# Kernel optimization log

Hardware: AMD Instinct MI355X
Metric: run time of the kernel (lower is better)

The kernel has to match this reference:

```python
import jax, jax.numpy as jnp
import numpy as np

NS, NV = 32, 8                      # scalar / vector multiplicities (32x0e + 8x1o)
N_NODES, N_EDGES = 16384, 131072
NEF, HID = 128, 128                 # edge feature dim, MLP hidden
WN = NS*NS + NV*NS + NS*NV + NV*NV  # 1600 tensor-product weights per edge
D = NS + 3*NV                       # 56 node feature dim
INV_SQRT3 = 1.0/np.sqrt(3.0)        # CG coeff for 1o x 1o -> 0e
PATH_NORM = 1.0/np.sqrt(NS + NV)    # fan-in normalization per output irrep
EPS = 1e-5


def setup_inputs() -> dict:
    key = jax.random.key(0)
    ks = jax.random.split(key, 10)
    node_attr = jax.random.normal(ks[0], (N_NODES, D), jnp.float32)
    edge_index = jax.random.randint(ks[1], (2, N_EDGES), 0, N_NODES, dtype=jnp.int64)
    edge_attr = jax.random.normal(ks[2], (N_EDGES, NEF), jnp.float32)
    edge_sh = jax.random.normal(ks[3], (N_EDGES, 4), jnp.float32)
    W1 = jax.random.normal(ks[4], (NEF, HID), jnp.float32) / np.sqrt(NEF)
    b1 = jnp.zeros((HID,), jnp.float32)
    W2 = jax.random.normal(ks[5], (HID, WN), jnp.float32) / np.sqrt(HID)
    b2 = jnp.zeros((WN,), jnp.float32)
    bn_gamma = jnp.ones((NS + NV,), jnp.float32)   # per-irrep scale (scalars then vectors)
    bn_beta = jnp.zeros((NS,), jnp.float32)        # bias only on scalar irreps
    return dict(node_attr=node_attr, edge_attr=edge_attr, edge_sh=edge_sh,
                W1=W1, b1=b1, W2=W2, b2=b2, bn_gamma=bn_gamma, bn_beta=bn_beta,
                edge_index=edge_index)


def reference(node_attr, edge_attr, edge_sh, W1, b1, W2, b2, bn_gamma, bn_beta, edge_index):
    edge_src, edge_dst = edge_index[0], edge_index[1]

    # per-edge tensor-product weights from edge MLP (dropout=0, eval mode)
    w = jax.nn.relu(edge_attr @ W1 + b1) @ W2 + b2            # [E, WN]
    o0 = NS*NS; o1 = o0 + NV*NS; o2 = o1 + NS*NV
    w_ss = w[:, :o0].reshape(-1, NS, NS)   # 0e x 0e -> 0e
    w_vs = w[:, o0:o1].reshape(-1, NV, NS) # 1o x 1o -> 0e
    w_sv = w[:, o1:o2].reshape(-1, NS, NV) # 0e x 1o -> 1o
    w_vv = w[:, o2:].reshape(-1, NV, NV)   # 1o x 0e -> 1o

    # gather node features onto edges
    x = node_attr[edge_dst]                # [E, D]
    xs = x[:, :NS]                         # [E, NS]
    xv = x[:, NS:].reshape(-1, NV, 3)      # [E, NV, 3]
    ss = edge_sh[:, 0]                     # [E]
    sv = edge_sh[:, 1:4]                   # [E, 3]

    # CG tensor product with per-edge fully-connected weights
    dot_vv = jnp.einsum('eim,em->ei', xv, sv) * INV_SQRT3
    out_s = (jnp.einsum('eij,ei->ej', w_ss, xs) * ss[:, None]
             + jnp.einsum('eij,ei->ej', w_vs, dot_vv)) * PATH_NORM          # [E, NS]
    out_v = (jnp.einsum('eij,ei->ej', w_sv, xs)[:, :, None] * sv[:, None, :]
             + jnp.einsum('eij,eim->ejm', w_vv, xv) * ss[:, None, None]) * PATH_NORM  # [E, NV, 3]
    tp = jnp.concatenate([out_s, out_v.reshape(-1, 3*NV)], axis=-1)         # [E, D]

    # scatter-mean to source nodes
    sums = jax.ops.segment_sum(tp, edge_src, num_segments=N_NODES)
    cnt = jax.ops.segment_sum(jnp.ones((tp.shape[0], 1), tp.dtype), edge_src,
                              num_segments=N_NODES)
    out = sums / jnp.maximum(cnt, 1.0)

    # residual (in/out irreps identical -> zero padding is a no-op)
    out = out + node_attr

    # equivariant batch norm (training-mode batch statistics)
    s = out[:, :NS]
    v = out[:, NS:].reshape(-1, NV, 3)
    s = (s - s.mean(0)) / jnp.sqrt(s.var(0) + EPS) * bn_gamma[:NS] + bn_beta
    vn2 = (v * v).sum(-1).mean(0)                               # [NV] mean squared norm
    v = v / jnp.sqrt(vn2 + EPS)[None, :, None] * bn_gamma[NS:][None, :, None]
    return jnp.concatenate([s, v.reshape(-1, 3*NV)], axis=-1)
```

## Files before the change

### kernel.cpp

```cpp
#include <hip/hip_runtime.h>

typedef short short8 __attribute__((ext_vector_type(8)));
typedef unsigned short us4 __attribute__((ext_vector_type(4)));
typedef float floatx4 __attribute__((ext_vector_type(4)));
typedef unsigned short u16;

#define NN 16384
#define NE 131072
#define NEF_ 128
#define DD 56
#define INV_SQRT3F 0.57735026918962576f
#define PATH_NORMF 0.15811388300841897f

__device__ __forceinline__ float bf2f(u16 u) {
    union { unsigned int i; float f; } v; v.i = ((unsigned int)u) << 16; return v.f;
}
__device__ __forceinline__ u16 f2bf(float f) {
    union { float f; unsigned int i; } v; v.f = f;
    unsigned int r = v.i + 0x7fffu + ((v.i >> 16) & 1u);
    return (u16)(r >> 16);
}

__global__ __launch_bounds__(256) void prep(const float* __restrict__ W1,
                                            const float* __restrict__ W2,
                                            u16* __restrict__ W1f,
                                            u16* __restrict__ W2f,
                                            const int* __restrict__ eidx,
                                            int* __restrict__ deg) {
    int b = blockIdx.x;
    if (b < 864) {
        int i = b * 256 + threadIdx.x;
        if (i < 16384) {
            int cc = i >> 13, kk = (i >> 11) & 3, cg = (i >> 9) & 3;
            int lane = (i >> 3) & 63, j = i & 7;
            int q = lane >> 4, m = lane & 15;
            W1f[i] = f2bf(W1[(kk * 32 + q * 8 + j) * 128 + cc * 64 + cg * 16 + m]);
        } else {
            int f = i - 16384;
            int c = f >> 13, kk = (f >> 11) & 3, cg = (f >> 9) & 3;
            int lane = (f >> 3) & 63, j = f & 7;
            int q = lane >> 4, m = lane & 15;
            W2f[f] = f2bf(W2[(kk * 32 + q * 8 + j) * 1600 + c * 64 + cg * 16 + m]);
        }
    } else {
        int e = (b - 864) * 256 + threadIdx.x;
        atomicAdd(&deg[eidx[e]], 1);
    }
}

__global__ __launch_bounds__(1024) void deg_scan(const int* __restrict__ deg,
                                                 int* __restrict__ row_start,
                                                 int* __restrict__ cursor) {
    __shared__ int part[1024];
    const int t = threadIdx.x;
    const int base = t * 16;
    int loc[16];
    int s = 0;
    #pragma unroll
    for (int i = 0; i < 16; i++) { loc[i] = s; s += deg[base + i]; }
    part[t] = s;
    __syncthreads();
    for (int off = 1; off < 1024; off <<= 1) {
        int v = (t >= off) ? part[t - off] : 0;
        __syncthreads();
        part[t] += v;
        __syncthreads();
    }
    int pre = (t == 0) ? 0 : part[t - 1];
    #pragma unroll
    for (int i = 0; i < 16; i++) {
        int v = pre + loc[i];
        row_start[base + i] = v;
        cursor[base + i] = v;
    }
    if (t == 1023) row_start[16384] = pre + s;
}

__global__ __launch_bounds__(256) void edge_scatter(const int* __restrict__ eidx,
                                                    int* __restrict__ cursor,
                                                    int* __restrict__ edge_order) {
    int e = blockIdx.x * 256 + threadIdx.x;
    int p = atomicAdd(&cursor[eidx[e]], 1);
    edge_order[p] = e;
}

__global__ __launch_bounds__(512, 4) void tpconv(
    const float* __restrict__ node_attr, const float* __restrict__ edge_attr,
    const float* __restrict__ edge_sh, const u16* __restrict__ W1f,
    const float* __restrict__ b1, const u16* __restrict__ W2f,
    const float* __restrict__ b2, const int* __restrict__ eidx,
    const int* __restrict__ edge_order,
    float* __restrict__ tp)
{
    __shared__ __align__(16) char smem[48896];
    u16*   sA  = (u16*)smem;
    u16*   B2a = (u16*)(smem + 17408);
    u16*   B2b = (u16*)smem;
    u16*   sF  = (u16*)(smem + 33792);
    float* b2s = (float*)(smem + 42496);
    float* Ssc  = (float*)smem;
    float* Svec = (float*)(smem + 16896);

    const int t = threadIdx.x;
    const int lane = t & 63;
    const int wv = t >> 6;
    const int m = lane & 15;
    const int q = lane >> 4;
    const int cg = wv & 3;
    const int eh = wv >> 2;
    const int eb = eh * 32;
    const int p0 = blockIdx.x * 64;

    short8 pre[2];
    #pragma unroll
    for (int ii = 0; ii < 2; ii++)
        pre[ii] = *(const short8*)&W2f[ii * 4096 + t * 8];

    for (int i = t; i < 1600; i += 512) b2s[i] = b2[i];

    #pragma unroll
    for (int ii = 0; ii < 4; ii++) {
        int cid = t + 512 * ii;
        int r = cid >> 5, s = cid & 31;
        int e = edge_order[p0 + r];
        const float* src = &edge_attr[(size_t)e * NEF_ + s * 4];
        us4 o;
        o.x = f2bf(src[0]); o.y = f2bf(src[1]); o.z = f2bf(src[2]); o.w = f2bf(src[3]);
        *(us4*)&sA[r * 136 + s * 4] = o;
    }
    if (t < 64) {
        int e = edge_order[p0 + t];
        int nd = eidx[NE + e];
        const float* na = node_attr + (size_t)nd * DD;
        const float* sh = edge_sh + (size_t)e * 4;
        float ss = sh[0], s0 = sh[1], s1 = sh[2], s2 = sh[3];
        #pragma unroll
        for (int i = 0; i < 32; i++) sF[i * 64 + t] = f2bf(na[i]);
        #pragma unroll
        for (int i = 0; i < 8; i++) {
            float d = (na[32+i*3]*s0 + na[33+i*3]*s1 + na[34+i*3]*s2) * INV_SQRT3F;
            sF[(32 + i) * 64 + t] = f2bf(d);
        }
        #pragma unroll
        for (int i = 0; i < 24; i++) sF[(40 + i) * 64 + t] = f2bf(na[32 + i]);
        sF[64 * 64 + t] = f2bf(ss);
        sF[65 * 64 + t] = f2bf(s0);
        sF[66 * 64 + t] = f2bf(s1);
        sF[67 * 64 + t] = f2bf(s2);
    }
    __syncthreads();

    floatx4 hacc[2][2];
    #pragma unroll
    for (int cc = 0; cc < 2; cc++) {
        #pragma unroll
        for (int ii = 0; ii < 2; ii++)
            *(short8*)&B2a[ii * 4096 + t * 8] =
                *(const short8*)&W1f[cc * 8192 + ii * 4096 + t * 8];
        __syncthreads();
        {
            float bv = b1[cc * 64 + cg * 16 + m];
            hacc[cc][0] = (floatx4){bv, bv, bv, bv};
            hacc[cc][1] = hacc[cc][0];
        }
        #pragma unroll
        for (int kk = 0; kk < 4; kk++) {
            short8 a0 = *(const short8*)&sA[(eb      + m) * 136 + kk * 32 + q * 8];
            short8 a1 = *(const short8*)&sA[(eb + 16 + m) * 136 + kk * 32 + q * 8];
            short8 bA = *(const short8*)&B2a[(kk * 4 + cg) * 512 + lane * 8];
            hacc[cc][0] = __builtin_amdgcn_mfma_f32_16x16x32_bf16(a0, bA, hacc[cc][0], 0, 0, 0);
            hacc[cc][1] = __builtin_amdgcn_mfma_f32_16x16x32_bf16(a1, bA, hacc[cc][1], 0, 0, 0);
        }
        __syncthreads();
    }
    #pragma unroll
    for (int cc = 0; cc < 2; cc++)
      #pragma unroll
      for (int rt = 0; rt < 2; rt++)
        #pragma unroll
        for (int r = 0; r < 4; r++) {
            int e   = eb + rt * 16 + q * 4 + r;
            int col = cc * 64 + cg * 16 + m;
            float v = hacc[cc][rt][r];
            sA[e * 136 + col] = f2bf(v > 0.f ? v : 0.f);
        }
    __syncthreads();

    short8 hc[2][4];
    #pragma unroll
    for (int et = 0; et < 2; et++)
        #pragma unroll
        for (int kk = 0; kk < 4; kk++)
            hc[et][kk] = *(const short8*)&sA[(eb + et * 16 + m) * 136 + kk * 32 + q * 8];

    float ssc[2], svc[2][3];
    #pragma unroll
    for (int et = 0; et < 2; et++) {
        ssc[et] = bf2f(sF[64 * 64 + eb + et * 16 + m]);
        svc[et][0] = bf2f(sF[65 * 64 + eb + et * 16 + m]);
        svc[et][1] = bf2f(sF[66 * 64 + eb + et * 16 + m]);
        svc[et][2] = bf2f(sF[67 * 64 + eb + et * 16 + m]);
    }

    #pragma unroll
    for (int ii = 0; ii < 2; ii++)
        *(short8*)&B2a[ii * 4096 + t * 8] = pre[ii];
    #pragma unroll
    for (int ii = 0; ii < 2; ii++)
        pre[ii] = *(const short8*)&W2f[8192 + ii * 4096 + t * 8];
    __syncthreads();

    float tps[2][4];
    float tpv[2][4][3];
    #pragma unroll
    for (int et = 0; et < 2; et++)
        #pragma unroll
        for (int r = 0; r < 4; r++) {
            tps[et][r] = 0.f;
            tpv[et][r][0] = 0.f; tpv[et][r][1] = 0.f; tpv[et][r][2] = 0.f;
        }

    for (int c = 0; c < 25; c++) {
        const u16* rb = (c & 1) ? B2b : B2a;
        u16*       wb = (c & 1) ? B2a : B2b;

        floatx4 bias = *(const floatx4*)&b2s[c * 64 + cg * 16 + q * 4];
        floatx4 acc[2];
        acc[0] = bias; acc[1] = bias;
        #pragma unroll
        for (int kk = 0; kk < 4; kk++) {
            short8 a = *(const short8*)&rb[(kk * 4 + cg) * 512 + lane * 8];
            acc[0] = __builtin_amdgcn_mfma_f32_16x16x32_bf16(a, hc[0][kk], acc[0], 0, 0, 0);
            acc[1] = __builtin_amdgcn_mfma_f32_16x16x32_bf16(a, hc[1][kk], acc[1], 0, 0, 0);
        }

        if (c < 24) {
            #pragma unroll
            for (int ii = 0; ii < 2; ii++)
                *(short8*)&wb[ii * 4096 + t * 8] = pre[ii];
            if (c < 23) {
                #pragma unroll
                for (int ii = 0; ii < 2; ii++)
                    pre[ii] = *(const short8*)&W2f[(size_t)(c + 2) * 8192 + ii * 4096 + t * 8];
            }
        }

        if (c < 16) {
            const int i = 2 * c + (cg >> 1);
            #pragma unroll
            for (int et = 0; et < 2; et++) {
                float f = bf2f(sF[i * 64 + eb + et * 16 + m]) * ssc[et];
                #pragma unroll
                for (int r = 0; r < 4; r++) tps[et][r] += acc[et][r] * f;
            }
        } else if (c < 20) {
            const int i = 2 * (c - 16) + (cg >> 1);
            #pragma unroll
            for (int et = 0; et < 2; et++) {
                float f = bf2f(sF[(32 + i) * 64 + eb + et * 16 + m]);
                #pragma unroll
                for (int r = 0; r < 4; r++) tps[et][r] += acc[et][r] * f;
            }
        } else if (c < 24) {
            const int i = 8 * (c - 20) + cg * 2 + (q >> 1);
            #pragma unroll
            for (int et = 0; et < 2; et++) {
                float f = bf2f(sF[i * 64 + eb + et * 16 + m]);
                #pragma unroll
                for (int r = 0; r < 4; r++) {
                    float t0 = acc[et][r] * f;
                    tpv[et][r][0] += t0 * svc[et][0];
                    tpv[et][r][1] += t0 * svc[et][1];
                    tpv[et][r][2] += t0 * svc[et][2];
                }
            }
        } else {
            const int i = cg * 2 + (q >> 1);
            #pragma unroll
            for (int et = 0; et < 2; et++) {
                float x0 = bf2f(sF[(40 + 3 * i + 0) * 64 + eb + et * 16 + m]) * ssc[et];
                float x1 = bf2f(sF[(40 + 3 * i + 1) * 64 + eb + et * 16 + m]) * ssc[et];
                float x2 = bf2f(sF[(40 + 3 * i + 2) * 64 + eb + et * 16 + m]) * ssc[et];
                #pragma unroll
                for (int r = 0; r < 4; r++) {
                    tpv[et][r][0] += acc[et][r] * x0;
                    tpv[et][r][1] += acc[et][r] * x1;
                    tpv[et][r][2] += acc[et][r] * x2;
                }
            }
        }

        __syncthreads();
    }

    #pragma unroll
    for (int et = 0; et < 2; et++)
        #pragma unroll
        for (int r = 0; r < 4; r++)
            Ssc[(cg >> 1) * 2112 + (eb + et * 16 + m) * 33 + (cg & 1) * 16 + q * 4 + r] = tps[et][r];
    #pragma unroll
    for (int et = 0; et < 2; et++)
        #pragma unroll
        for (int r = 0; r < 4; r++)
            #pragma unroll
            for (int mm = 0; mm < 3; mm++) {
                float v = tpv[et][r][mm];
                v += __shfl_xor(v, 32, 64);
                if (q < 2)
                    Svec[cg * 1600 + (eb + et * 16 + m) * 25 + ((q & 1) * 4 + r) * 3 + mm] = v;
            }
    __syncthreads();

    for (int idx = t; idx < 3584; idx += 512) {
        int e = idx / 56, d = idx - e * 56;
        float v;
        if (d < 32) {
            v = Ssc[e * 33 + d] + Ssc[2112 + e * 33 + d];
        } else {
            int dd = d - 32;
            v = Svec[e * 25 + dd] + Svec[1600 + e * 25 + dd]
              + Svec[3200 + e * 25 + dd] + Svec[4800 + e * 25 + dd];
        }
        tp[(size_t)(p0 + e) * DD + d] = v * PATH_NORMF;
    }
}

__global__ __launch_bounds__(256) void gather_finalize(
    const float* __restrict__ tp, const int* __restrict__ row_start,
    const float* __restrict__ node_attr,
    float* __restrict__ ybuf, float* __restrict__ partial)
{
    __shared__ float ps[4][72];
    const int wv = threadIdx.x >> 6, lane = threadIdx.x & 63;
    const int n = blockIdx.x * 4 + wv;
    const int beg = row_start[n], end = row_start[n + 1];
    if (lane < 56) {
        float acc = 0.f;
        for (int p = beg; p < end; p++)
            acc += tp[(size_t)p * DD + lane];
        float inv = 1.f / fmaxf((float)(end - beg), 1.f);
        float y = acc * inv + node_attr[(size_t)n * DD + lane];
        ybuf[(size_t)n * DD + lane] = y;
        if (lane < 32) {
            ps[wv][lane] = y;
            ps[wv][32 + lane] = y * y;
        } else {
            float vv = y * y;
            float v1 = __shfl_down(vv, 1, 64);
            float v2 = __shfl_down(vv, 2, 64);
            int l3 = lane - 32;
            if (l3 % 3 == 0) ps[wv][64 + l3 / 3] = vv + v1 + v2;
        }
    }
    __syncthreads();
    const int t = threadIdx.x;
    if (t < 72)
        partial[(size_t)blockIdx.x * 72 + t] = ps[0][t] + ps[1][t] + ps[2][t] + ps[3][t];
}

__global__ __launch_bounds__(256) void bn_reduce(const float* __restrict__ partial,
                                                 float* __restrict__ stats)
{
    __shared__ float red[256];
    const int d = blockIdx.x;
    const int t = threadIdx.x;
    float a = 0.f;
    for (int i = t; i < 4096; i += 256) a += partial[(size_t)i * 72 + d];
    red[t] = a;
    __syncthreads();
    for (int off = 128; off > 0; off >>= 1) {
        if (t < off) red[t] += red[t + off];
        __syncthreads();
    }
    if (t == 0) stats[d] = red[0] * (1.f / 16384.f);
}

__global__ __launch_bounds__(256) void bn_apply(
    const float* __restrict__ ybuf, const float* __restrict__ stats,
    const float* __restrict__ gamma, const float* __restrict__ beta,
    float* __restrict__ out)
{
    const int i = blockIdx.x * 256 + threadIdx.x;
    const int n = i / 56;
    const int d = i - n * 56;
    float y = ybuf[i];
    float o;
    if (d < 32) {
        float mn  = stats[d];
        float var = stats[32 + d] - mn * mn;
        o = (y - mn) * rsqrtf(var + 1e-5f) * gamma[d] + beta[d];
    } else {
        int jv = (d - 32) / 3;
        o = y * rsqrtf(stats[64 + jv] + 1e-5f) * gamma[32 + jv];
    }
    out[i] = o;
}

extern "C" void kernel_launch(void* const* d_in, const int* in_sizes, int n_in,
                              void* d_out, int out_size, void* d_ws, size_t ws_size,
                              hipStream_t stream)
{
    const float* node_attr = (const float*)d_in[0];
    const float* edge_attr = (const float*)d_in[1];
    const float* edge_sh   = (const float*)d_in[2];
    const float* W1        = (const float*)d_in[3];
    const float* b1        = (const float*)d_in[4];
    const float* W2        = (const float*)d_in[5];
    const float* b2        = (const float*)d_in[6];
    const float* gamma     = (const float*)d_in[7];
    const float* beta      = (const float*)d_in[8];
    const int*   eidx      = (const int*)d_in[9];

    char* ws = (char*)d_ws;
    u16*   W1f        = (u16*)(ws);
    u16*   W2f        = (u16*)(ws + 32768);
    int*   deg        = (int*)(ws + 442368);
    int*   row_start  = (int*)(ws + 507904);
    int*   cursor     = (int*)(ws + 573696);
    int*   edge_order = (int*)(ws + 639232);
    float* stats      = (float*)(ws + 1163520);
    float* partial    = (float*)(ws + 1164032);
    float* tp         = (float*)(ws + 2343680);
    float* ybuf       = (float*)(ws + 31703808);

    (void)hipMemsetAsync(deg, 0, 65536, stream);
    hipLaunchKernelGGL(prep,            dim3(1376), dim3(256),  0, stream,
                       W1, W2, W1f, W2f, eidx, deg);
    hipLaunchKernelGGL(deg_scan,        dim3(1),    dim3(1024), 0, stream, deg, row_start, cursor);
    hipLaunchKernelGGL(edge_scatter,    dim3(512),  dim3(256),  0, stream, eidx, cursor, edge_order);
    hipLaunchKernelGGL(tpconv,          dim3(2048), dim3(512),  0, stream,
                       node_attr, edge_attr, edge_sh, W1f, b1, W2f, b2, eidx, edge_order, tp);
    hipLaunchKernelGGL(gather_finalize, dim3(4096), dim3(256),  0, stream,
                       tp, row_start, node_attr, ybuf, partial);
    hipLaunchKernelGGL(bn_reduce,       dim3(72),   dim3(256),  0, stream, partial, stats);
    hipLaunchKernelGGL(bn_apply,        dim3(3584), dim3(256),  0, stream,
                       ybuf, stats, gamma, beta, (float*)d_out);
}
```

Measured before the change: 248.8 us.

## Use direct global-to-LDS loads for weights and spread node gather across all waves

Weight tiles for W1 and W2 are now streamed straight into shared memory with global_load_lds, replacing the register prefetch and store path. This removes register pressure and the extra LDS store instructions, and the next W2 chunk is issued at the top of each iteration. The node-feature gather, which previously ran serially on the first 64 threads, is now split across all eight waves with coalesced per-lane loads, at the cost of one extra barrier. Correctness depends on the async LDS writes being complete at the existing barriers, and the LDS offsets rely on wave-uniform addressing.

```diff
diff --git a/kernel.cpp b/kernel.cpp
--- a/kernel.cpp
+++ b/kernel.cpp
@@ -11,6 +11,11 @@
 #define DD 56
 #define INV_SQRT3F 0.57735026918962576f
 #define PATH_NORMF 0.15811388300841897f
+
+#define G2L(gsrc, ldst)                                                           \
+    __builtin_amdgcn_global_load_lds(                                             \
+        (const __attribute__((address_space(1))) void*)(gsrc),                    \
+        (__attribute__((address_space(3))) void*)(ldst), 16, 0, 0)
 
 __device__ __forceinline__ float bf2f(u16 u) {
     union { unsigned int i; float f; } v; v.i = ((unsigned int)u) << 16; return v.f;
@@ -93,6 +98,8 @@
     float* __restrict__ tp)
 {
     __shared__ __align__(16) char smem[48896];
+    __shared__ int sND[64];
+    __shared__ float sSH[4 * 64];
     u16*   sA  = (u16*)smem;
     u16*   B2a = (u16*)(smem + 17408);
     u16*   B2b = (u16*)smem;
@@ -111,10 +118,9 @@
     const int eb = eh * 32;
     const int p0 = blockIdx.x * 64;
 
-    short8 pre[2];
     #pragma unroll
     for (int ii = 0; ii < 2; ii++)
-        pre[ii] = *(const short8*)&W2f[ii * 4096 + t * 8];
+        G2L(&W1f[ii * 4096 + t * 8], &B2a[ii * 4096 + wv * 512]);
 
     for (int i = t; i < 1600; i += 512) b2s[i] = b2[i];
 
@@ -130,19 +136,11 @@
     }
     if (t < 64) {
         int e = edge_order[p0 + t];
-        int nd = eidx[NE + e];
-        const float* na = node_attr + (size_t)nd * DD;
+        sND[t] = eidx[NE + e];
         const float* sh = edge_sh + (size_t)e * 4;
         float ss = sh[0], s0 = sh[1], s1 = sh[2], s2 = sh[3];
-        #pragma unroll
-        for (int i = 0; i < 32; i++) sF[i * 64 + t] = f2bf(na[i]);
-        #pragma unroll
-        for (int i = 0; i < 8; i++) {
-            float d = (na[32+i*3]*s0 + na[33+i*3]*s1 + na[34+i*3]*s2) * INV_SQRT3F;
-            sF[(32 + i) * 64 + t] = f2bf(d);
-        }
-        #pragma unroll
-        for (int i = 0; i < 24; i++) sF[(40 + i) * 64 + t] = f2bf(na[32 + i]);
+        sSH[0 * 64 + t] = ss; sSH[1 * 64 + t] = s0;
+        sSH[2 * 64 + t] = s1; sSH[3 * 64 + t] = s2;
         sF[64 * 64 + t] = f2bf(ss);
         sF[65 * 64 + t] = f2bf(s0);
         sF[66 * 64 + t] = f2bf(s1);
@@ -150,14 +148,27 @@
     }
     __syncthreads();
 
+    const int nd = sND[lane];
+    #pragma unroll
+    for (int ii = 0; ii < 7; ii++) {
+        int d = wv + 8 * ii;
+        float v = node_attr[(size_t)nd * DD + d];
+        int row = (d < 32) ? d : (40 + d - 32);
+        sF[row * 64 + lane] = f2bf(v);
+    }
+    {
+        float x0 = node_attr[(size_t)nd * DD + 32 + 3 * wv + 0];
+        float x1 = node_attr[(size_t)nd * DD + 32 + 3 * wv + 1];
+        float x2 = node_attr[(size_t)nd * DD + 32 + 3 * wv + 2];
+        float d = (x0 * sSH[1 * 64 + lane] + x1 * sSH[2 * 64 + lane]
+                 + x2 * sSH[3 * 64 + lane]) * INV_SQRT3F;
+        sF[(32 + wv) * 64 + lane] = f2bf(d);
+    }
+    __syncthreads();
+
     floatx4 hacc[2][2];
     #pragma unroll
     for (int cc = 0; cc < 2; cc++) {
-        #pragma unroll
-        for (int ii = 0; ii < 2; ii++)
-            *(short8*)&B2a[ii * 4096 + t * 8] =
-                *(const short8*)&W1f[cc * 8192 + ii * 4096 + t * 8];
-        __syncthreads();
         {
             float bv = b1[cc * 64 + cg * 16 + m];
             hacc[cc][0] = (floatx4){bv, bv, bv, bv};
@@ -172,6 +183,12 @@
             hacc[cc][1] = __builtin_amdgcn_mfma_f32_16x16x32_bf16(a1, bA, hacc[cc][1], 0, 0, 0);
         }
         __syncthreads();
+        if (cc == 0) {
+            #pragma unroll
+            for (int ii = 0; ii < 2; ii++)
+                G2L(&W1f[8192 + ii * 4096 + t * 8], &B2a[ii * 4096 + wv * 512]);
+            __syncthreads();
+        }
     }
     #pragma unroll
     for (int cc = 0; cc < 2; cc++)
@@ -204,10 +221,7 @@
 
     #pragma unroll
     for (int ii = 0; ii < 2; ii++)
-        *(short8*)&B2a[ii * 4096 + t * 8] = pre[ii];
-    #pragma unroll
-    for (int ii = 0; ii < 2; ii++)
-        pre[ii] = *(const short8*)&W2f[8192 + ii * 4096 + t * 8];
+        G2L(&W2f[ii * 4096 + t * 8], &B2a[ii * 4096 + wv * 512]);
     __syncthreads();
 
     float tps[2][4];
@@ -222,7 +236,12 @@
 
     for (int c = 0; c < 25; c++) {
         const u16* rb = (c & 1) ? B2b : B2a;
-        u16*       wb = (c & 1) ? B2a : B2b;
+        if (c < 24) {
+            u16* wb = (c & 1) ? B2a : B2b;
+            #pragma unroll
+            for (int ii = 0; ii < 2; ii++)
+                G2L(&W2f[(size_t)(c + 1) * 8192 + ii * 4096 + t * 8], &wb[ii * 4096 + wv * 512]);
+        }
 
         floatx4 bias = *(const floatx4*)&b2s[c * 64 + cg * 16 + q * 4];
         floatx4 acc[2];
@@ -232,17 +251,6 @@
             short8 a = *(const short8*)&rb[(kk * 4 + cg) * 512 + lane * 8];
             acc[0] = __builtin_amdgcn_mfma_f32_16x16x32_bf16(a, hc[0][kk], acc[0], 0, 0, 0);
             acc[1] = __builtin_amdgcn_mfma_f32_16x16x32_bf16(a, hc[1][kk], acc[1], 0, 0, 0);
-        }
-
-        if (c < 24) {
-            #pragma unroll
-            for (int ii = 0; ii < 2; ii++)
-                *(short8*)&wb[ii * 4096 + t * 8] = pre[ii];
-            if (c < 23) {
-                #pragma unroll
-                for (int ii = 0; ii < 2; ii++)
-                    pre[ii] = *(const short8*)&W2f[(size_t)(c + 2) * 8192 + ii * 4096 + t * 8];
-            }
         }
 
         if (c < 16) {
```

After: 453.6 us. 1.82x slower.
